# Performance work log

Hardware: AMD Instinct MI355X
Metric: run time of the kernel (lower is better)

## Reference

```python
import math
import jax, jax.numpy as jnp
import numpy as np

B, S, H, E, F = 4, 2048, 1024, 8, 2048
CAPACITY_FACTOR = 1.25


def setup_inputs() -> dict:
    key = jax.random.key(0)
    ks = jax.random.split(key, 5)
    x = jax.random.normal(ks[0], (B, S, H), dtype=jnp.float32)
    gate_w = jax.random.normal(ks[1], (H, E), dtype=jnp.float32) * 0.02
    w1 = jax.random.normal(ks[2], (E, H, F), dtype=jnp.float32) * 0.02
    w2 = jax.random.normal(ks[3], (E, F, H), dtype=jnp.float32) * 0.02
    w3 = jax.random.normal(ks[4], (E, H, F), dtype=jnp.float32) * 0.02
    return {"x": x, "gate_w": gate_w, "w1": w1, "w2": w2, "w3": w3}


def reference(x, gate_w, w1, w2, w3):
    b, s, h = x.shape
    T = b * s
    e = gate_w.shape[1]
    xf = x.reshape(T, h)                           # [T, H]
    logits = xf @ gate_w                           # [T, E]
    capacity = min(math.ceil(T / e * CAPACITY_FACTOR), T)
    # Expert-choice: each expert picks its top-`capacity` tokens.
    scores, idx = jax.lax.top_k(logits.T, capacity)  # both [E, C]
    # Per-expert softmax over the selected tokens (dim=0 of the column vector in torch == capacity axis here).
    weights = jax.nn.softmax(scores, axis=1)       # [E, C]
    gathered = xf[idx]                             # [E, C, H]
    # Grouped SwiGLU FFN
    a = jnp.einsum('ech,ehf->ecf', gathered, w1)
    g = jnp.einsum('ech,ehf->ecf', gathered, w3)
    hidden = jax.nn.silu(a) * g                    # [E, C, F]
    out_e = jnp.einsum('ecf,efh->ech', hidden, w2) # [E, C, H]
    out_e = out_e * weights[..., None]
    # Weighted scatter-add combine
    yf = jnp.zeros((T, h), dtype=x.dtype).at[idx.reshape(-1)].add(
        out_e.reshape(-1, h))
    return yf.reshape(b, s, h), jnp.float32(0.0)
```

## Files before the change

### kernel.cpp

```cpp
#include <hip/hip_runtime.h>
#include <stdint.h>

typedef unsigned short ushort_t;
typedef __bf16 bf16x8 __attribute__((ext_vector_type(8)));
typedef float f32x4 __attribute__((ext_vector_type(4)));

#define T_TOK 8192
#define HDIM  1024
#define EXP   8
#define FDIM  2048
#define CAP   1280

__device__ __forceinline__ unsigned short f2b(float f) {
  unsigned u = __float_as_uint(f);
  u = (u + 0x7fffu + ((u >> 16) & 1u)) >> 16;
  return (unsigned short)u;
}
__device__ __forceinline__ unsigned pk2(unsigned short lo, unsigned short hi) {
  return (unsigned)lo | ((unsigned)hi << 16);
}
__device__ __forceinline__ unsigned map_u(float f) {
  unsigned u = __float_as_uint(f);
  return (u & 0x80000000u) ? ~u : (u | 0x80000000u);
}
__device__ __forceinline__ float unmap_f(unsigned m) {
  unsigned u = (m & 0x80000000u) ? (m ^ 0x80000000u) : ~m;
  return __uint_as_float(u);
}
__device__ __forceinline__ void gl_lds16(const void* g, void* l) {
  __builtin_amdgcn_global_load_lds((__attribute__((address_space(1))) void*)g,
                                   (__attribute__((address_space(3))) void*)l,
                                   16, 0, 0);
}

__global__ void __launch_bounds__(256) gate_cast_k(
    const float* __restrict__ x, const float* __restrict__ gw,
    float* __restrict__ logitsT, ushort_t* __restrict__ xb)
{
  int wave = threadIdx.x >> 6, lane = threadIdx.x & 63;
  int t = blockIdx.x * 4 + wave;
  const float* xr = x + (size_t)t * HDIM;
  ushort_t* xbr = xb + (size_t)t * HDIM;
  float acc[8];
#pragma unroll
  for (int i = 0; i < 8; ++i) acc[i] = 0.f;
#pragma unroll
  for (int i = 0; i < 4; ++i) {
    int h0 = i * 256 + lane * 4;
    float4 xv = *(const float4*)(xr + h0);
    unsigned lo = pk2(f2b(xv.x), f2b(xv.y));
    unsigned hi = pk2(f2b(xv.z), f2b(xv.w));
    *(unsigned long long*)(xbr + h0) = (unsigned long long)lo | ((unsigned long long)hi << 32);
    float xs[4] = {xv.x, xv.y, xv.z, xv.w};
#pragma unroll
    for (int j = 0; j < 4; ++j) {
      const float4* g4 = (const float4*)(gw + (size_t)(h0 + j) * EXP);
      float4 glo = g4[0], ghi = g4[1];
      acc[0] += xs[j] * glo.x; acc[1] += xs[j] * glo.y;
      acc[2] += xs[j] * glo.z; acc[3] += xs[j] * glo.w;
      acc[4] += xs[j] * ghi.x; acc[5] += xs[j] * ghi.y;
      acc[6] += xs[j] * ghi.z; acc[7] += xs[j] * ghi.w;
    }
  }
#pragma unroll
  for (int off = 32; off > 0; off >>= 1) {
#pragma unroll
    for (int i = 0; i < 8; ++i) acc[i] += __shfl_xor(acc[i], off, 64);
  }
  if (lane == 0) {
#pragma unroll
    for (int i = 0; i < 8; ++i) logitsT[(size_t)i * T_TOK + t] = acc[i];
  }
}

__global__ void __launch_bounds__(256) select_k(
    const float* __restrict__ logitsT,
    unsigned* __restrict__ thr, int* __restrict__ needo, unsigned* __restrict__ umax)
{
  __shared__ int hist[4][256];
  __shared__ int ssum[256];
  __shared__ unsigned s_pref;
  __shared__ int s_rem;
  __shared__ unsigned smx[4];
  int e = blockIdx.x, tid = threadIdx.x;
  const float* base = logitsT + (size_t)e * T_TOK;

  unsigned m[32];
  unsigned mmax = 0;
#pragma unroll
  for (int i = 0; i < 32; ++i) {
    m[i] = map_u(base[tid + i * 256]);
    mmax = m[i] > mmax ? m[i] : mmax;
  }
#pragma unroll
  for (int off = 32; off > 0; off >>= 1) {
    unsigned o = __shfl_xor(mmax, off, 64);
    mmax = o > mmax ? o : mmax;
  }
  int lane = tid & 63, wv = tid >> 6;
  if (lane == 0) smx[wv] = mmax;
  if (tid == 0) { s_pref = 0; s_rem = CAP; }
  __syncthreads();
  if (tid == 0) {
    unsigned a = smx[0] > smx[1] ? smx[0] : smx[1];
    unsigned b = smx[2] > smx[3] ? smx[2] : smx[3];
    umax[e] = a > b ? a : b;
  }

  for (int r = 0; r < 4; ++r) {
#pragma unroll
    for (int w = 0; w < 4; ++w) hist[w][tid] = 0;
    __syncthreads();
    unsigned pref = s_pref;
    int rem = s_rem;
    int shift = 24 - 8 * r;
#pragma unroll
    for (int i = 0; i < 32; ++i) {
      unsigned u = m[i];
      bool ok = (r == 0) || ((u >> (shift + 8)) == (pref >> (shift + 8)));
      if (ok) atomicAdd(&hist[wv][(u >> shift) & 255], 1);
    }
    __syncthreads();
    ssum[tid] = hist[0][tid] + hist[1][tid] + hist[2][tid] + hist[3][tid];
    __syncthreads();
    for (int st = 1; st < 256; st <<= 1) {
      int add = (tid + st < 256) ? ssum[tid + st] : 0;
      __syncthreads();
      ssum[tid] += add;
      __syncthreads();
    }
    int above = (tid < 255) ? ssum[tid + 1] : 0;
    if (ssum[tid] >= rem && above < rem) {
      s_pref = pref | ((unsigned)tid << shift);
      s_rem = rem - above;
    }
    __syncthreads();
  }
  if (tid == 0) { thr[e] = s_pref; needo[e] = s_rem; }
}

__global__ void __launch_bounds__(256) emit_k(
    const float* __restrict__ logitsT,
    const unsigned* __restrict__ thr, const int* __restrict__ needv,
    const unsigned* __restrict__ umaxv,
    int* __restrict__ idxo, float* __restrict__ exo,
    int* __restrict__ cnt, int* __restrict__ tie, float* __restrict__ expsum,
    int* __restrict__ tok_cnt, int* __restrict__ tok_ent)
{
  int t = blockIdx.x * 256 + threadIdx.x;
  int lane = threadIdx.x & 63;
  int lc = 0;
  int ents[8];
#pragma unroll
  for (int e = 0; e < EXP; ++e) {
    float f = logitsT[(size_t)e * T_TOK + t];
    unsigned u = map_u(f);
    unsigned te = thr[e];
    float fm = unmap_f(umaxv[e]);
    float v = __expf(f - fm);
    bool sel = u > te;
    unsigned long long mask = __ballot(sel);
    int nsel = __popcll(mask);
    int base = 0;
    if (lane == 0 && nsel) base = atomicAdd(&cnt[e], nsel);
    base = __shfl(base, 0, 64);
    int slot = -1;
    if (sel) slot = base + __popcll(mask & ((1ull << lane) - 1ull));
    if (u == te) {
      int k = atomicAdd(&tie[e], 1);
      if (k < needv[e]) {
        slot = atomicAdd(&cnt[e], 1);
        atomicAdd(&expsum[e], v);
      }
    }
    if (slot >= 0) {
      idxo[e * CAP + slot] = t;
      exo[e * CAP + slot] = v;
      ents[lc++] = (e << 16) | slot;
    }
    float vs = sel ? v : 0.f;
#pragma unroll
    for (int off = 32; off > 0; off >>= 1) vs += __shfl_xor(vs, off, 64);
    if (lane == 0 && vs != 0.f) atomicAdd(&expsum[e], vs);
  }
  tok_cnt[t] = lc;
  for (int i = 0; i < lc; ++i) tok_ent[t * 8 + i] = ents[i];
}

__global__ void __launch_bounds__(256) transpose3_k(
    const float* __restrict__ w1, const float* __restrict__ w3, const float* __restrict__ w2,
    ushort_t* __restrict__ w1t, ushort_t* __restrict__ w3t, ushort_t* __restrict__ w2t)
{
  __shared__ float tile[64][65];
  int b = blockIdx.x;
  const float* in; ushort_t* out; int R, Cc;
  if (b < 4096)      { in = w1; out = w1t; R = HDIM; Cc = FDIM; }
  else if (b < 8192) { in = w3; out = w3t; R = HDIM; Cc = FDIM; b -= 4096; }
  else               { in = w2; out = w2t; R = FDIM; Cc = HDIM; b -= 8192; }
  int tilesC = Cc >> 6;
  int tilesPer = (R >> 6) * tilesC;
  int e = b / tilesPer;
  int tb = b - e * tilesPer;
  int rt = tb / tilesC, ct = tb - rt * tilesC;
  const float* src = in + (size_t)e * R * Cc;
  ushort_t* dst = out + (size_t)e * R * Cc;
  int tr = threadIdx.x >> 4, tc = threadIdx.x & 15;
#pragma unroll
  for (int it = 0; it < 4; ++it) {
    int r = (rt << 6) + (it << 4) + tr;
    int c = (ct << 6) + (tc << 2);
    float4 v = *(const float4*)(src + (size_t)r * Cc + c);
    tile[(it << 4) + tr][(tc << 2) + 0] = v.x;
    tile[(it << 4) + tr][(tc << 2) + 1] = v.y;
    tile[(it << 4) + tr][(tc << 2) + 2] = v.z;
    tile[(it << 4) + tr][(tc << 2) + 3] = v.w;
  }
  __syncthreads();
#pragma unroll
  for (int it = 0; it < 4; ++it) {
    int cl = (it << 4) + tr;
    int rl = tc << 2;
    unsigned lo = pk2(f2b(tile[rl + 0][cl]), f2b(tile[rl + 1][cl]));
    unsigned hi = pk2(f2b(tile[rl + 2][cl]), f2b(tile[rl + 3][cl]));
    unsigned long long v = (unsigned long long)lo | ((unsigned long long)hi << 32);
    *(unsigned long long*)(dst + (size_t)((ct << 6) + cl) * R + (rt << 6) + rl) = v;
  }
}

#define G1_STAGE(BB) \
  gl_lds16(pA0, lds + (BB)*12288 + (size_t)tid*8); \
  gl_lds16(pA1, lds + (BB)*12288 + 4096 + (size_t)tid*8); \
  gl_lds16(pB , lds + (BB)*12288 + 8192 + (size_t)tid*8);

#define G1_ITER(CB, PB, VM, PREF) { \
  asm volatile("s_waitcnt vmcnt(" VM ")" ::: "memory"); \
  __builtin_amdgcn_s_barrier(); \
  if (PREF) { G1_STAGE(PB); pA0 += 32; pA1 += 32; pB += 32; } \
  bf16x8 af[4], b1v[2], b3v[2]; \
  _Pragma("unroll") \
  for (int mi = 0; mi < 4; ++mi) af[mi] = *(const bf16x8*)(lds + (CB)*12288 + aoff[mi]); \
  _Pragma("unroll") \
  for (int nj = 0; nj < 2; ++nj) { \
    b1v[nj] = *(const bf16x8*)(lds + (CB)*12288 + b1off[nj]); \
    b3v[nj] = *(const bf16x8*)(lds + (CB)*12288 + b1off[nj] + 2048); } \
  __builtin_amdgcn_s_setprio(1); \
  _Pragma("unroll") \
  for (int mi = 0; mi < 4; ++mi) \
    _Pragma("unroll") \
    for (int nj = 0; nj < 2; ++nj) { \
      acc1[mi][nj] = __builtin_amdgcn_mfma_f32_16x16x32_bf16(af[mi], b1v[nj], acc1[mi][nj], 0, 0, 0); \
      acc3[mi][nj] = __builtin_amdgcn_mfma_f32_16x16x32_bf16(af[mi], b3v[nj], acc3[mi][nj], 0, 0, 0); } \
  __builtin_amdgcn_s_setprio(0); \
}

__global__ void __launch_bounds__(512) gemm1_swiglu_k(
    const ushort_t* __restrict__ xb,
    const ushort_t* __restrict__ w1t,
    const ushort_t* __restrict__ w3t,
    const int* __restrict__ idx,
    ushort_t* __restrict__ hidden)
{
  int bb = blockIdx.x;
  int b = (bb & 7) * 160 + (bb >> 3);
  int ft = b & 31; int t1 = b >> 5; int mt = t1 % 5; int e = t1 / 5;
  int f0 = ft * 64;

  __shared__ __bf16 lds[3 * 12288];

  int tid = threadIdx.x;
  int lane = tid & 63, wave = tid >> 6;
  int wm = wave >> 1;
  int wn = wave & 1;
  int l15 = lane & 15, quad = lane >> 4;

  int srow = tid >> 2;
  int chunk = tid & 3;
  int s_sw = (srow & 3) ^ ((srow >> 2) & 3);
  int g_chunk = ((chunk ^ s_sw) * 8);

  const int* idxe = idx + e * CAP + mt * 256;
  int tok0 = idxe[srow];
  int tok1 = idxe[srow + 128];
  const ushort_t* pA0 = xb + (size_t)tok0 * HDIM + g_chunk;
  const ushort_t* pA1 = xb + (size_t)tok1 * HDIM + g_chunk;
  const ushort_t* pB = (srow < 64)
      ? (w1t + ((size_t)e * FDIM + f0 + srow) * HDIM + g_chunk)
      : (w3t + ((size_t)e * FDIM + f0 + (srow - 64)) * HDIM + g_chunk);

  int aoff[4], b1off[2];
#pragma unroll
  for (int mi = 0; mi < 4; ++mi) {
    int R = wm * 64 + mi * 16 + l15;
    int sw = (R & 3) ^ ((R >> 2) & 3);
    aoff[mi] = R * 32 + ((quad ^ sw) * 8);
  }
#pragma unroll
  for (int nj = 0; nj < 2; ++nj) {
    int r1 = wn * 32 + nj * 16 + l15;
    int sw = (r1 & 3) ^ ((r1 >> 2) & 3);
    b1off[nj] = 8192 + r1 * 32 + ((quad ^ sw) * 8);
  }

  f32x4 acc1[4][2], acc3[4][2];
#pragma unroll
  for (int i = 0; i < 4; ++i)
#pragma unroll
    for (int j = 0; j < 2; ++j) {
      acc1[i][j] = (f32x4){0.f, 0.f, 0.f, 0.f};
      acc3[i][j] = (f32x4){0.f, 0.f, 0.f, 0.f};
    }

  G1_STAGE(0); pA0 += 32; pA1 += 32; pB += 32;
  G1_STAGE(1); pA0 += 32; pA1 += 32; pB += 32;

  for (int it = 0; it < 10; ++it) {
    G1_ITER(0, 2, "3", 1)
    G1_ITER(1, 0, "3", 1)
    G1_ITER(2, 1, "3", 1)
  }
  G1_ITER(0, 0, "3", 0)
  G1_ITER(1, 0, "0", 0)

  ushort_t* hb = hidden + ((size_t)e * CAP + mt * 256) * FDIM + f0;
#pragma unroll
  for (int mi = 0; mi < 4; ++mi)
#pragma unroll
    for (int nj = 0; nj < 2; ++nj)
#pragma unroll
      for (int r = 0; r < 4; ++r) {
        int row = wm * 64 + mi * 16 + quad * 4 + r;
        int col = wn * 32 + nj * 16 + l15;
        float v1 = acc1[mi][nj][r];
        float v3 = acc3[mi][nj][r];
        float s = (v1 / (1.f + __expf(-v1))) * v3;
        hb[(size_t)row * FDIM + col] = f2b(s);
      }
}

#define G2_STAGE(BB) \
  gl_lds16(pA, lds2 + (BB)*8192 + (size_t)tid*8); \
  gl_lds16(pB, lds2 + (BB)*8192 + 4096 + (size_t)tid*8);

#define G2_ITER(CB, PB, VM, PREF) { \
  asm volatile("s_waitcnt vmcnt(" VM ")" ::: "memory"); \
  __builtin_amdgcn_s_barrier(); \
  if (PREF) { G2_STAGE(PB); pA += 32; pB += 32; } \
  bf16x8 af[4], bf[2]; \
  _Pragma("unroll") \
  for (int mi = 0; mi < 4; ++mi) af[mi] = *(const bf16x8*)(lds2 + (CB)*8192 + aoff[mi]); \
  _Pragma("unroll") \
  for (int nj = 0; nj < 2; ++nj) bf[nj] = *(const bf16x8*)(lds2 + (CB)*8192 + boff[nj]); \
  __builtin_amdgcn_s_setprio(1); \
  _Pragma("unroll") \
  for (int mi = 0; mi < 4; ++mi) \
    _Pragma("unroll") \
    for (int nj = 0; nj < 2; ++nj) \
      acc[mi][nj] = __builtin_amdgcn_mfma_f32_16x16x32_bf16(af[mi], bf[nj], acc[mi][nj], 0, 0, 0); \
  __builtin_amdgcn_s_setprio(0); \
}

__global__ void __launch_bounds__(512) gemm2_k(
    const ushort_t* __restrict__ hidden,
    const ushort_t* __restrict__ w2t,
    const float* __restrict__ ex, const float* __restrict__ expsum,
    float* __restrict__ oute)
{
  int bb = blockIdx.x;
  int b = (bb & 7) * 80 + (bb >> 3);
  int nt = b & 7; int t1 = b >> 3; int mt = t1 % 10; int e = t1 / 10;

  __shared__ __bf16 lds2[3 * 8192];
  __shared__ float wgts[128];

  int tid = threadIdx.x;
  int lane = tid & 63, wave = tid >> 6;
  int wm = wave >> 2;
  int wn = wave & 3;
  int l15 = lane & 15, quad = lane >> 4;

  if (tid < 128) wgts[tid] = ex[e * CAP + mt * 128 + tid] / expsum[e];

  int srow = tid >> 2;
  int chunk = tid & 3;
  int s_sw = (srow & 3) ^ ((srow >> 2) & 3);
  int g_chunk = ((chunk ^ s_sw) * 8);

  const ushort_t* pA = hidden + ((size_t)e * CAP + mt * 128 + srow) * FDIM + g_chunk;
  const ushort_t* pB = w2t + ((size_t)e * HDIM + nt * 128 + srow) * FDIM + g_chunk;

  int aoff[4], boff[2];
#pragma unroll
  for (int mi = 0; mi < 4; ++mi) {
    int R = wm * 64 + mi * 16 + l15;
    int sw = (R & 3) ^ ((R >> 2) & 3);
    aoff[mi] = R * 32 + ((quad ^ sw) * 8);
  }
#pragma unroll
  for (int nj = 0; nj < 2; ++nj) {
    int r = wn * 32 + nj * 16 + l15;
    int sw = (r & 3) ^ ((r >> 2) & 3);
    boff[nj] = 4096 + r * 32 + ((quad ^ sw) * 8);
  }

  f32x4 acc[4][2];
#pragma unroll
  for (int i = 0; i < 4; ++i)
#pragma unroll
    for (int j = 0; j < 2; ++j) acc[i][j] = (f32x4){0.f, 0.f, 0.f, 0.f};

  G2_STAGE(0); pA += 32; pB += 32;
  G2_STAGE(1); pA += 32; pB += 32;

  for (int it = 0; it < 20; ++it) {
    G2_ITER(0, 2, "2", 1)
    G2_ITER(1, 0, "2", 1)
    G2_ITER(2, 1, "2", 1)
  }
  G2_ITER(0, 2, "2", 1)
  G2_ITER(1, 0, "2", 1)
  G2_ITER(2, 0, "2", 0)
  G2_ITER(0, 0, "0", 0)

  float* ob = oute + ((size_t)e * CAP + mt * 128) * HDIM + nt * 128;
#pragma unroll
  for (int mi = 0; mi < 4; ++mi)
#pragma unroll
    for (int nj = 0; nj < 2; ++nj)
#pragma unroll
      for (int r = 0; r < 4; ++r) {
        int row = wm * 64 + mi * 16 + quad * 4 + r;
        int col = wn * 32 + nj * 16 + l15;
        ob[(size_t)row * HDIM + col] = acc[mi][nj][r] * wgts[row];
      }
}

__global__ void __launch_bounds__(256) combine_k(
    const float* __restrict__ oute,
    const int* __restrict__ tok_cnt, const int* __restrict__ tok_ent,
    float* __restrict__ y)
{
  int t = blockIdx.x;
  int c = threadIdx.x * 4;
  int n = tok_cnt[t];
  float4 acc = {0.f, 0.f, 0.f, 0.f};
  for (int i = 0; i < n; ++i) {
    int ent = tok_ent[t * 8 + i];
    int e = ent >> 16, slot = ent & 0xffff;
    float4 v = *(const float4*)(oute + (((size_t)e * CAP + slot) << 10) + c);
    acc.x += v.x; acc.y += v.y; acc.z += v.z; acc.w += v.w;
  }
  *(float4*)(y + ((size_t)t << 10) + c) = acc;
}

extern "C" void kernel_launch(void* const* d_in, const int* in_sizes, int n_in,
                              void* d_out, int out_size, void* d_ws, size_t ws_size,
                              hipStream_t stream)
{
  const float* x  = (const float*)d_in[0];
  const float* gw = (const float*)d_in[1];
  const float* w1 = (const float*)d_in[2];
  const float* w2 = (const float*)d_in[3];
  const float* w3 = (const float*)d_in[4];
  float* y = (float*)d_out;

  char* ws = (char*)d_ws;
  float*    logitsT = (float*)(ws + 0x0);
  int*      idx     = (int*)(ws + 0x40000);
  float*    exo     = (float*)(ws + 0x4A000);
  unsigned* thr    = (unsigned*)(ws + 0x54000);
  int*      need   = (int*)(ws + 0x54020);
  unsigned* umax   = (unsigned*)(ws + 0x54040);
  int*      cnt    = (int*)(ws + 0x54060);
  int*      tie    = (int*)(ws + 0x54080);
  float*    expsum = (float*)(ws + 0x540A0);
  int*      tok_cnt = (int*)(ws + 0x55000);
  int*      tok_ent = (int*)(ws + 0x5D000);
  ushort_t* xb     = (ushort_t*)(ws + 0xA0000);
  ushort_t* w1t    = (ushort_t*)(ws + 0x10A0000);
  ushort_t* w3t    = (ushort_t*)(ws + 0x30A0000);
  ushort_t* w2t    = (ushort_t*)(ws + 0x50A0000);
  ushort_t* hid    = (ushort_t*)(ws + 0x70A0000);
  float*    oute   = (float*)(ws + 0x10A0000);

  size_t yelems = (size_t)T_TOK * HDIM;
  if ((size_t)out_size > yelems)
    hipMemsetAsync((char*)d_out + yelems * 4, 0, ((size_t)out_size - yelems) * 4, stream);
  hipMemsetAsync(ws + 0x54000, 0, 256, stream);

  transpose3_k<<<3 * 4096, 256, 0, stream>>>(w1, w3, w2, w1t, w3t, w2t);
  gate_cast_k<<<T_TOK / 4, 256, 0, stream>>>(x, gw, logitsT, xb);
  select_k<<<EXP, 256, 0, stream>>>(logitsT, thr, need, umax);
  emit_k<<<T_TOK / 256, 256, 0, stream>>>(logitsT, thr, need, umax, idx, exo, cnt, tie, expsum, tok_cnt, tok_ent);
  gemm1_swiglu_k<<<EXP * 5 * 32, 512, 0, stream>>>(xb, w1t, w3t, idx, hid);
  gemm2_k<<<EXP * 10 * 8, 512, 0, stream>>>(hid, w2t, exo, expsum, oute);
  combine_k<<<T_TOK, 256, 0, stream>>>(oute, tok_cnt, tok_ent, y);
}
```

Measured before the change: 468.9 us.

## Merge transpose and gate kernels; shrink gemm1 tiles to 128 rows

Folds the weight transpose/cast kernel and the gate/cast kernel into one launch, with block ranges selecting the role. This removes a launch and lets the two independent prep stages overlap. The SwiGLU gemm1 moves from 512-thread blocks on 256-token tiles to 256-thread blocks on 128-token tiles, with a smaller LDS footprint and twice the grid. The block-to-tile mapping is also changed to interleave experts. Smaller tiles mean more weight reloads per token but higher occupancy and more blocks to spread across CUs.

After: 475.5 us. Within noise of the previous version (+1.4%).

```diff
diff --git a/kernel.cpp b/kernel.cpp
--- a/kernel.cpp
+++ b/kernel.cpp
@@ -33,43 +33,83 @@
                                    16, 0, 0);
 }
 
-__global__ void __launch_bounds__(256) gate_cast_k(
+__global__ void __launch_bounds__(256) prep_k(
+    const float* __restrict__ w1, const float* __restrict__ w3, const float* __restrict__ w2,
+    ushort_t* __restrict__ w1t, ushort_t* __restrict__ w3t, ushort_t* __restrict__ w2t,
     const float* __restrict__ x, const float* __restrict__ gw,
     float* __restrict__ logitsT, ushort_t* __restrict__ xb)
 {
-  int wave = threadIdx.x >> 6, lane = threadIdx.x & 63;
-  int t = blockIdx.x * 4 + wave;
-  const float* xr = x + (size_t)t * HDIM;
-  ushort_t* xbr = xb + (size_t)t * HDIM;
-  float acc[8];
-#pragma unroll
-  for (int i = 0; i < 8; ++i) acc[i] = 0.f;
-#pragma unroll
-  for (int i = 0; i < 4; ++i) {
-    int h0 = i * 256 + lane * 4;
-    float4 xv = *(const float4*)(xr + h0);
-    unsigned lo = pk2(f2b(xv.x), f2b(xv.y));
-    unsigned hi = pk2(f2b(xv.z), f2b(xv.w));
-    *(unsigned long long*)(xbr + h0) = (unsigned long long)lo | ((unsigned long long)hi << 32);
-    float xs[4] = {xv.x, xv.y, xv.z, xv.w};
-#pragma unroll
-    for (int j = 0; j < 4; ++j) {
-      const float4* g4 = (const float4*)(gw + (size_t)(h0 + j) * EXP);
-      float4 glo = g4[0], ghi = g4[1];
-      acc[0] += xs[j] * glo.x; acc[1] += xs[j] * glo.y;
-      acc[2] += xs[j] * glo.z; acc[3] += xs[j] * glo.w;
-      acc[4] += xs[j] * ghi.x; acc[5] += xs[j] * ghi.y;
-      acc[6] += xs[j] * ghi.z; acc[7] += xs[j] * ghi.w;
-    }
-  }
-#pragma unroll
-  for (int off = 32; off > 0; off >>= 1) {
-#pragma unroll
-    for (int i = 0; i < 8; ++i) acc[i] += __shfl_xor(acc[i], off, 64);
-  }
-  if (lane == 0) {
-#pragma unroll
-    for (int i = 0; i < 8; ++i) logitsT[(size_t)i * T_TOK + t] = acc[i];
+  __shared__ float tile[64][65];
+  int bb = blockIdx.x;
+  if (bb >= 12288) {
+    int wave = threadIdx.x >> 6, lane = threadIdx.x & 63;
+    int t = (bb - 12288) * 4 + wave;
+    const float* xr = x + (size_t)t * HDIM;
+    ushort_t* xbr = xb + (size_t)t * HDIM;
+    float acc[8];
+#pragma unroll
+    for (int i = 0; i < 8; ++i) acc[i] = 0.f;
+#pragma unroll
+    for (int i = 0; i < 4; ++i) {
+      int h0 = i * 256 + lane * 4;
+      float4 xv = *(const float4*)(xr + h0);
+      unsigned lo = pk2(f2b(xv.x), f2b(xv.y));
+      unsigned hi = pk2(f2b(xv.z), f2b(xv.w));
+      *(unsigned long long*)(xbr + h0) = (unsigned long long)lo | ((unsigned long long)hi << 32);
+      float xs[4] = {xv.x, xv.y, xv.z, xv.w};
+#pragma unroll
+      for (int j = 0; j < 4; ++j) {
+        const float4* g4 = (const float4*)(gw + (size_t)(h0 + j) * EXP);
+        float4 glo = g4[0], ghi = g4[1];
+        acc[0] += xs[j] * glo.x; acc[1] += xs[j] * glo.y;
+        acc[2] += xs[j] * glo.z; acc[3] += xs[j] * glo.w;
+        acc[4] += xs[j] * ghi.x; acc[5] += xs[j] * ghi.y;
+        acc[6] += xs[j] * ghi.z; acc[7] += xs[j] * ghi.w;
+      }
+    }
+#pragma unroll
+    for (int off = 32; off > 0; off >>= 1) {
+#pragma unroll
+      for (int i = 0; i < 8; ++i) acc[i] += __shfl_xor(acc[i], off, 64);
+    }
+    if (lane == 0) {
+#pragma unroll
+      for (int i = 0; i < 8; ++i) logitsT[(size_t)i * T_TOK + t] = acc[i];
+    }
+    return;
+  }
+  int b = bb;
+  const float* in; ushort_t* out; int R, Cc;
+  if (b < 4096)      { in = w1; out = w1t; R = HDIM; Cc = FDIM; }
+  else if (b < 8192) { in = w3; out = w3t; R = HDIM; Cc = FDIM; b -= 4096; }
+  else               { in = w2; out = w2t; R = FDIM; Cc = HDIM; b -= 8192; }
+  int tilesC = Cc >> 6;
+  int tilesPer = (R >> 6) * tilesC;
+  int e = b / tilesPer;
+  int tb = b - e * tilesPer;
+  int rt = tb / tilesC, ct = tb - rt * tilesC;
+  const float* src = in + (size_t)e * R * Cc;
+  ushort_t* dst = out + (size_t)e * R * Cc;
+  int tr = threadIdx.x >> 4, tc = threadIdx.x & 15;
+#pragma unroll
+  for (int it = 0; it < 4; ++it) {
+    int r = (rt << 6) + (it << 4) + tr;
+    int c = (ct << 6) + (tc << 2);
+    float4 v = *(const float4*)(src + (size_t)r * Cc + c);
+    tile[(it << 4) + tr][(tc << 2) + 0] = v.x;
+    tile[(it << 4) + tr][(tc << 2) + 1] = v.y;
+    tile[(it << 4) + tr][(tc << 2) + 2] = v.z;
+    tile[(it << 4) + tr][(tc << 2) + 3] = v.w;
+  }
+  __syncthreads();
+#pragma unroll
+  for (int it = 0; it < 4; ++it) {
+    int cl = (it << 4) + tr;
+    int rl = tc << 2;
+    unsigned lo = pk2(f2b(tile[rl + 0][cl]), f2b(tile[rl + 1][cl]));
+    unsigned hi = pk2(f2b(tile[rl + 2][cl]), f2b(tile[rl + 3][cl]));
+    unsigned long long v = (unsigned long long)lo | ((unsigned long long)hi << 32);
+    *(unsigned long long*)(dst + (size_t)((ct << 6) + cl) * R + (rt << 6) + rl) = v;
   }
 }
 
@@ -187,62 +227,25 @@
   for (int i = 0; i < lc; ++i) tok_ent[t * 8 + i] = ents[i];
 }
 
-__global__ void __launch_bounds__(256) transpose3_k(
-    const float* __restrict__ w1, const float* __restrict__ w3, const float* __restrict__ w2,
-    ushort_t* __restrict__ w1t, ushort_t* __restrict__ w3t, ushort_t* __restrict__ w2t)
-{
-  __shared__ float tile[64][65];
-  int b = blockIdx.x;
-  const float* in; ushort_t* out; int R, Cc;
-  if (b < 4096)      { in = w1; out = w1t; R = HDIM; Cc = FDIM; }
-  else if (b < 8192) { in = w3; out = w3t; R = HDIM; Cc = FDIM; b -= 4096; }
-  else               { in = w2; out = w2t; R = FDIM; Cc = HDIM; b -= 8192; }
-  int tilesC = Cc >> 6;
-  int tilesPer = (R >> 6) * tilesC;
-  int e = b / tilesPer;
-  int tb = b - e * tilesPer;
-  int rt = tb / tilesC, ct = tb - rt * tilesC;
-  const float* src = in + (size_t)e * R * Cc;
-  ushort_t* dst = out + (size_t)e * R * Cc;
-  int tr = threadIdx.x >> 4, tc = threadIdx.x & 15;
-#pragma unroll
-  for (int it = 0; it < 4; ++it) {
-    int r = (rt << 6) + (it << 4) + tr;
-    int c = (ct << 6) + (tc << 2);
-    float4 v = *(const float4*)(src + (size_t)r * Cc + c);
-    tile[(it << 4) + tr][(tc << 2) + 0] = v.x;
-    tile[(it << 4) + tr][(tc << 2) + 1] = v.y;
-    tile[(it << 4) + tr][(tc << 2) + 2] = v.z;
-    tile[(it << 4) + tr][(tc << 2) + 3] = v.w;
-  }
-  __syncthreads();
-#pragma unroll
-  for (int it = 0; it < 4; ++it) {
-    int cl = (it << 4) + tr;
-    int rl = tc << 2;
-    unsigned lo = pk2(f2b(tile[rl + 0][cl]), f2b(tile[rl + 1][cl]));
-    unsigned hi = pk2(f2b(tile[rl + 2][cl]), f2b(tile[rl + 3][cl]));
-    unsigned long long v = (unsigned long long)lo | ((unsigned long long)hi << 32);
-    *(unsigned long long*)(dst + (size_t)((ct << 6) + cl) * R + (rt << 6) + rl) = v;
-  }
-}
-
 #define G1_STAGE(BB) \
-  gl_lds16(pA0, lds + (BB)*12288 + (size_t)tid*8); \
-  gl_lds16(pA1, lds + (BB)*12288 + 4096 + (size_t)tid*8); \
-  gl_lds16(pB , lds + (BB)*12288 + 8192 + (size_t)tid*8);
-
-#define G1_ITER(CB, PB, VM, PREF) { \
+  gl_lds16(pA0, lds + (BB)*8192 + (size_t)tid*8); \
+  gl_lds16(pA1, lds + (BB)*8192 + 2048 + (size_t)tid*8); \
+  gl_lds16(pB0, lds + (BB)*8192 + 4096 + (size_t)tid*8); \
+  gl_lds16(pB1, lds + (BB)*8192 + 6144 + (size_t)tid*8);
+
+#define G1_ADV { pA0 += 32; pA1 += 32; pB0 += 32; pB1 += 32; }
+
+#define G1_ITER(CB, VM, PREF) { \
   asm volatile("s_waitcnt vmcnt(" VM ")" ::: "memory"); \
   __builtin_amdgcn_s_barrier(); \
-  if (PREF) { G1_STAGE(PB); pA0 += 32; pA1 += 32; pB += 32; } \
+  if (PREF) { G1_STAGE(((CB) + 2) % 3); G1_ADV; } \
   bf16x8 af[4], b1v[2], b3v[2]; \
   _Pragma("unroll") \
-  for (int mi = 0; mi < 4; ++mi) af[mi] = *(const bf16x8*)(lds + (CB)*12288 + aoff[mi]); \
+  for (int mi = 0; mi < 4; ++mi) af[mi] = *(const bf16x8*)(lds + (CB)*8192 + aoff[mi]); \
   _Pragma("unroll") \
   for (int nj = 0; nj < 2; ++nj) { \
-    b1v[nj] = *(const bf16x8*)(lds + (CB)*12288 + b1off[nj]); \
-    b3v[nj] = *(const bf16x8*)(lds + (CB)*12288 + b1off[nj] + 2048); } \
+    b1v[nj] = *(const bf16x8*)(lds + (CB)*8192 + b1off[nj]); \
+    b3v[nj] = *(const bf16x8*)(lds + (CB)*8192 + b1off[nj] + 2048); } \
   __builtin_amdgcn_s_setprio(1); \
   _Pragma("unroll") \
   for (int mi = 0; mi < 4; ++mi) \
@@ -253,7 +256,7 @@
   __builtin_amdgcn_s_setprio(0); \
 }
 
-__global__ void __launch_bounds__(512) gemm1_swiglu_k(
+__global__ void __launch_bounds__(256) gemm1_swiglu_k(
     const ushort_t* __restrict__ xb,
     const ushort_t* __restrict__ w1t,
     const ushort_t* __restrict__ w3t,
@@ -261,11 +264,13 @@
     ushort_t* __restrict__ hidden)
 {
   int bb = blockIdx.x;
-  int b = (bb & 7) * 160 + (bb >> 3);
-  int ft = b & 31; int t1 = b >> 5; int mt = t1 % 5; int e = t1 / 5;
+  int e = bb & 7;
+  int k = bb >> 3;
+  int mt = k % 10;
+  int ft = k / 10;
   int f0 = ft * 64;
 
-  __shared__ __bf16 lds[3 * 12288];
+  __shared__ __bf16 lds[3 * 8192];
 
   int tid = threadIdx.x;
   int lane = tid & 63, wave = tid >> 6;
@@ -273,19 +278,18 @@
   int wn = wave & 1;
   int l15 = lane & 15, quad = lane >> 4;
 
-  int srow = tid >> 2;
-  int chunk = tid & 3;
-  int s_sw = (srow & 3) ^ ((srow >> 2) & 3);
-  int g_chunk = ((chunk ^ s_sw) * 8);
-
-  const int* idxe = idx + e * CAP + mt * 256;
-  int tok0 = idxe[srow];
-  int tok1 = idxe[srow + 128];
+  int r = tid >> 2;
+  int c = tid & 3;
+  int s_sw = (r & 3) ^ ((r >> 2) & 3);
+  int g_chunk = ((c ^ s_sw) * 8);
+
+  const int* idxe = idx + e * CAP + mt * 128;
+  int tok0 = idxe[r];
+  int tok1 = idxe[r + 64];
   const ushort_t* pA0 = xb + (size_t)tok0 * HDIM + g_chunk;
   const ushort_t* pA1 = xb + (size_t)tok1 * HDIM + g_chunk;
-  const ushort_t* pB = (srow < 64)
-      ? (w1t + ((size_t)e * FDIM + f0 + srow) * HDIM + g_chunk)
-      : (w3t + ((size_t)e * FDIM + f0 + (srow - 64)) * HDIM + g_chunk);
+  const ushort_t* pB0 = w1t + ((size_t)e * FDIM + f0 + r) * HDIM + g_chunk;
+  const ushort_t* pB1 = w3t + ((size_t)e * FDIM + f0 + r) * HDIM + g_chunk;
 
   int aoff[4], b1off[2];
 #pragma unroll
@@ -298,7 +302,7 @@
   for (int nj = 0; nj < 2; ++nj) {
     int r1 = wn * 32 + nj * 16 + l15;
     int sw = (r1 & 3) ^ ((r1 >> 2) & 3);
-    b1off[nj] = 8192 + r1 * 32 + ((quad ^ sw) * 8);
+    b1off[nj] = 4096 + r1 * 32 + ((quad ^ sw) * 8);
   }
 
   f32x4 acc1[4][2], acc3[4][2];
@@ -310,28 +314,28 @@
       acc3[i][j] = (f32x4){0.f, 0.f, 0.f, 0.f};
     }
 
-  G1_STAGE(0); pA0 += 32; pA1 += 32; pB += 32;
-  G1_STAGE(1); pA0 += 32; pA1 += 32; pB += 32;
+  G1_STAGE(0); G1_ADV;
+  G1_STAGE(1); G1_ADV;
 
   for (int it = 0; it < 10; ++it) {
-    G1_ITER(0, 2, "3", 1)
-    G1_ITER(1, 0, "3", 1)
-    G1_ITER(2, 1, "3", 1)
-  }
-  G1_ITER(0, 0, "3", 0)
-  G1_ITER(1, 0, "0", 0)
-
-  ushort_t* hb = hidden + ((size_t)e * CAP + mt * 256) * FDIM + f0;
+    G1_ITER(0, "4", 1)
+    G1_ITER(1, "4", 1)
+    G1_ITER(2, "4", 1)
+  }
+  G1_ITER(0, "4", 0)
+  G1_ITER(1, "0", 0)
+
+  ushort_t* hb = hidden + ((size_t)e * CAP + mt * 128) * FDIM + f0;
 #pragma unroll
   for (int mi = 0; mi < 4; ++mi)
 #pragma unroll
     for (int nj = 0; nj < 2; ++nj)
 #pragma unroll
-      for (int r = 0; r < 4; ++r) {
-        int row = wm * 64 + mi * 16 + quad * 4 + r;
+      for (int rr = 0; rr < 4; ++rr) {
+        int row = wm * 64 + mi * 16 + quad * 4 + rr;
         int col = wn * 32 + nj * 16 + l15;
-        float v1 = acc1[mi][nj][r];
-        float v3 = acc3[mi][nj][r];
+        float v1 = acc1[mi][nj][rr];
+        float v3 = acc3[mi][nj][rr];
         float s = (v1 / (1.f + __expf(-v1))) * v3;
         hb[(size_t)row * FDIM + col] = f2b(s);
       }
@@ -397,9 +401,9 @@
   }
 #pragma unroll
   for (int nj = 0; nj < 2; ++nj) {
-    int r = wn * 32 + nj * 16 + l15;
-    int sw = (r & 3) ^ ((r >> 2) & 3);
-    boff[nj] = 4096 + r * 32 + ((quad ^ sw) * 8);
+    int r2 = wn * 32 + nj * 16 + l15;
+    int sw = (r2 & 3) ^ ((r2 >> 2) & 3);
+    boff[nj] = 4096 + r2 * 32 + ((quad ^ sw) * 8);
   }
 
   f32x4 acc[4][2];
@@ -427,10 +431,10 @@
 #pragma unroll
     for (int nj = 0; nj < 2; ++nj)
 #pragma unroll
-      for (int r = 0; r < 4; ++r) {
-        int row = wm * 64 + mi * 16 + quad * 4 + r;
+      for (int rr = 0; rr < 4; ++rr) {
+        int row = wm * 64 + mi * 16 + quad * 4 + rr;
         int col = wn * 32 + nj * 16 + l15;
-        ob[(size_t)row * HDIM + col] = acc[mi][nj][r] * wgts[row];
+        ob[(size_t)row * HDIM + col] = acc[mi][nj][rr] * wgts[row];
       }
 }
 
@@ -487,11 +491,10 @@
     hipMemsetAsync((char*)d_out + yelems * 4, 0, ((size_t)out_size - yelems) * 4, stream);
   hipMemsetAsync(ws + 0x54000, 0, 256, stream);
 
-  transpose3_k<<<3 * 4096, 256, 0, stream>>>(w1, w3, w2, w1t, w3t, w2t);
-  gate_cast_k<<<T_TOK / 4, 256, 0, stream>>>(x, gw, logitsT, xb);
+  prep_k<<<12288 + 2048, 256, 0, stream>>>(w1, w3, w2, w1t, w3t, w2t, x, gw, logitsT, xb);
   select_k<<<EXP, 256, 0, stream>>>(logitsT, thr, need, umax);
   emit_k<<<T_TOK / 256, 256, 0, stream>>>(logitsT, thr, need, umax, idx, exo, cnt, tie, expsum, tok_cnt, tok_ent);
-  gemm1_swiglu_k<<<EXP * 5 * 32, 512, 0, stream>>>(xb, w1t, w3t, idx, hid);
+  gemm1_swiglu_k<<<EXP * 10 * 32, 256, 0, stream>>>(xb, w1t, w3t, idx, hid);
   gemm2_k<<<EXP * 10 * 8, 512, 0, stream>>>(hid, w2t, exo, expsum, oute);
   combine_k<<<T_TOK, 256, 0, stream>>>(oute, tok_cnt, tok_ent, y);
 }
```

## Merge weight transpose and gate/cast kernels; transpose four tiles per block

Applied to the files above, without the earlier changes.

Combines the weight transpose-to-bf16 kernel and the gate-logit/x-cast kernel into one launch, with block ranges dispatched to each role. Each transpose block now handles four 64x64 tiles, issuing all global loads before the LDS transposes so more memory requests are in flight. The goal is to cut one launch plus its tail and raise memory-level parallelism. In exchange each transpose block holds more registers and has fewer blocks to spread the work. Some loop variables in gemm2 are also renamed with no effect.

Result: no change. 465.9 us (-0.6%).

```diff
diff --git a/kernel.cpp b/kernel.cpp
--- a/kernel.cpp
+++ b/kernel.cpp
@@ -33,44 +33,102 @@
                                    16, 0, 0);
 }
 
-__global__ void __launch_bounds__(256) gate_cast_k(
+#define PREP_LOAD(VV, G) { \
+  _Pragma("unroll") \
+  for (int it = 0; it < 4; ++it) { \
+    int r = (rt << 6) + (it << 4) + tr; \
+    int c = ((ct0 + (G)) << 6) + (tc << 2); \
+    VV[it] = *(const float4*)(src + (size_t)r * Cc + c); \
+  } }
+
+#define PREP_DO(VV, G) { \
+  __syncthreads(); \
+  _Pragma("unroll") \
+  for (int it = 0; it < 4; ++it) { \
+    tile[(it << 4) + tr][(tc << 2) + 0] = VV[it].x; \
+    tile[(it << 4) + tr][(tc << 2) + 1] = VV[it].y; \
+    tile[(it << 4) + tr][(tc << 2) + 2] = VV[it].z; \
+    tile[(it << 4) + tr][(tc << 2) + 3] = VV[it].w; \
+  } \
+  __syncthreads(); \
+  _Pragma("unroll") \
+  for (int it = 0; it < 4; ++it) { \
+    int cl = (it << 4) + tr; \
+    int rl = tc << 2; \
+    unsigned lo = pk2(f2b(tile[rl + 0][cl]), f2b(tile[rl + 1][cl])); \
+    unsigned hi = pk2(f2b(tile[rl + 2][cl]), f2b(tile[rl + 3][cl])); \
+    unsigned long long v = (unsigned long long)lo | ((unsigned long long)hi << 32); \
+    *(unsigned long long*)(dst + (size_t)(((ct0 + (G)) << 6) + cl) * R + (rt << 6) + rl) = v; \
+  } }
+
+__global__ void __launch_bounds__(256) prep_k(
+    const float* __restrict__ w1, const float* __restrict__ w3, const float* __restrict__ w2,
+    ushort_t* __restrict__ w1t, ushort_t* __restrict__ w3t, ushort_t* __restrict__ w2t,
     const float* __restrict__ x, const float* __restrict__ gw,
     float* __restrict__ logitsT, ushort_t* __restrict__ xb)
 {
-  int wave = threadIdx.x >> 6, lane = threadIdx.x & 63;
-  int t = blockIdx.x * 4 + wave;
-  const float* xr = x + (size_t)t * HDIM;
-  ushort_t* xbr = xb + (size_t)t * HDIM;
-  float acc[8];
-#pragma unroll
-  for (int i = 0; i < 8; ++i) acc[i] = 0.f;
-#pragma unroll
-  for (int i = 0; i < 4; ++i) {
-    int h0 = i * 256 + lane * 4;
-    float4 xv = *(const float4*)(xr + h0);
-    unsigned lo = pk2(f2b(xv.x), f2b(xv.y));
-    unsigned hi = pk2(f2b(xv.z), f2b(xv.w));
-    *(unsigned long long*)(xbr + h0) = (unsigned long long)lo | ((unsigned long long)hi << 32);
-    float xs[4] = {xv.x, xv.y, xv.z, xv.w};
-#pragma unroll
-    for (int j = 0; j < 4; ++j) {
-      const float4* g4 = (const float4*)(gw + (size_t)(h0 + j) * EXP);
-      float4 glo = g4[0], ghi = g4[1];
-      acc[0] += xs[j] * glo.x; acc[1] += xs[j] * glo.y;
-      acc[2] += xs[j] * glo.z; acc[3] += xs[j] * glo.w;
-      acc[4] += xs[j] * ghi.x; acc[5] += xs[j] * ghi.y;
-      acc[6] += xs[j] * ghi.z; acc[7] += xs[j] * ghi.w;
-    }
-  }
-#pragma unroll
-  for (int off = 32; off > 0; off >>= 1) {
-#pragma unroll
-    for (int i = 0; i < 8; ++i) acc[i] += __shfl_xor(acc[i], off, 64);
-  }
-  if (lane == 0) {
-#pragma unroll
-    for (int i = 0; i < 8; ++i) logitsT[(size_t)i * T_TOK + t] = acc[i];
-  }
+  __shared__ float tile[64][65];
+  int bb = blockIdx.x;
+  if (bb >= 3072) {
+    int wave = threadIdx.x >> 6, lane = threadIdx.x & 63;
+    int t = (bb - 3072) * 4 + wave;
+    const float* xr = x + (size_t)t * HDIM;
+    ushort_t* xbr = xb + (size_t)t * HDIM;
+    float acc[8];
+#pragma unroll
+    for (int i = 0; i < 8; ++i) acc[i] = 0.f;
+#pragma unroll
+    for (int i = 0; i < 4; ++i) {
+      int h0 = i * 256 + lane * 4;
+      float4 xv = *(const float4*)(xr + h0);
+      unsigned lo = pk2(f2b(xv.x), f2b(xv.y));
+      unsigned hi = pk2(f2b(xv.z), f2b(xv.w));
+      *(unsigned long long*)(xbr + h0) = (unsigned long long)lo | ((unsigned long long)hi << 32);
+      float xs[4] = {xv.x, xv.y, xv.z, xv.w};
+#pragma unroll
+      for (int j = 0; j < 4; ++j) {
+        const float4* g4 = (const float4*)(gw + (size_t)(h0 + j) * EXP);
+        float4 glo = g4[0], ghi = g4[1];
+        acc[0] += xs[j] * glo.x; acc[1] += xs[j] * glo.y;
+        acc[2] += xs[j] * glo.z; acc[3] += xs[j] * glo.w;
+        acc[4] += xs[j] * ghi.x; acc[5] += xs[j] * ghi.y;
+        acc[6] += xs[j] * ghi.z; acc[7] += xs[j] * ghi.w;
+      }
+    }
+#pragma unroll
+    for (int off = 32; off > 0; off >>= 1) {
+#pragma unroll
+      for (int i = 0; i < 8; ++i) acc[i] += __shfl_xor(acc[i], off, 64);
+    }
+    if (lane == 0) {
+#pragma unroll
+      for (int i = 0; i < 8; ++i) logitsT[(size_t)i * T_TOK + t] = acc[i];
+    }
+    return;
+  }
+  int b = bb;
+  const float* in; ushort_t* out; int R, Cc;
+  if (b < 1024)      { in = w1; out = w1t; R = HDIM; Cc = FDIM; }
+  else if (b < 2048) { in = w3; out = w3t; R = HDIM; Cc = FDIM; b -= 1024; }
+  else               { in = w2; out = w2t; R = FDIM; Cc = HDIM; b -= 2048; }
+  int colgroups = Cc >> 8;
+  int e = b >> 7;
+  int tb = b & 127;
+  int rt = tb / colgroups;
+  int ct0 = (tb % colgroups) * 4;
+  const float* src = in + (size_t)e * R * Cc;
+  ushort_t* dst = out + (size_t)e * R * Cc;
+  int tr = threadIdx.x >> 4, tc = threadIdx.x & 15;
+
+  float4 v0[4], v1[4], v2[4], v3[4];
+  PREP_LOAD(v0, 0)
+  PREP_LOAD(v1, 1)
+  PREP_LOAD(v2, 2)
+  PREP_LOAD(v3, 3)
+  PREP_DO(v0, 0)
+  PREP_DO(v1, 1)
+  PREP_DO(v2, 2)
+  PREP_DO(v3, 3)
 }
 
 __global__ void __launch_bounds__(256) select_k(
@@ -187,46 +245,6 @@
   for (int i = 0; i < lc; ++i) tok_ent[t * 8 + i] = ents[i];
 }
 
-__global__ void __launch_bounds__(256) transpose3_k(
-    const float* __restrict__ w1, const float* __restrict__ w3, const float* __restrict__ w2,
-    ushort_t* __restrict__ w1t, ushort_t* __restrict__ w3t, ushort_t* __restrict__ w2t)
-{
-  __shared__ float tile[64][65];
-  int b = blockIdx.x;
-  const float* in; ushort_t* out; int R, Cc;
-  if (b < 4096)      { in = w1; out = w1t; R = HDIM; Cc = FDIM; }
-  else if (b < 8192) { in = w3; out = w3t; R = HDIM; Cc = FDIM; b -= 4096; }
-  else               { in = w2; out = w2t; R = FDIM; Cc = HDIM; b -= 8192; }
-  int tilesC = Cc >> 6;
-  int tilesPer = (R >> 6) * tilesC;
-  int e = b / tilesPer;
-  int tb = b - e * tilesPer;
-  int rt = tb / tilesC, ct = tb - rt * tilesC;
-  const float* src = in + (size_t)e * R * Cc;
-  ushort_t* dst = out + (size_t)e * R * Cc;
-  int tr = threadIdx.x >> 4, tc = threadIdx.x & 15;
-#pragma unroll
-  for (int it = 0; it < 4; ++it) {
-    int r = (rt << 6) + (it << 4) + tr;
-    int c = (ct << 6) + (tc << 2);
-    float4 v = *(const float4*)(src + (size_t)r * Cc + c);
-    tile[(it << 4) + tr][(tc << 2) + 0] = v.x;
-    tile[(it << 4) + tr][(tc << 2) + 1] = v.y;
-    tile[(it << 4) + tr][(tc << 2) + 2] = v.z;
-    tile[(it << 4) + tr][(tc << 2) + 3] = v.w;
-  }
-  __syncthreads();
-#pragma unroll
-  for (int it = 0; it < 4; ++it) {
-    int cl = (it << 4) + tr;
-    int rl = tc << 2;
-    unsigned lo = pk2(f2b(tile[rl + 0][cl]), f2b(tile[rl + 1][cl]));
-    unsigned hi = pk2(f2b(tile[rl + 2][cl]), f2b(tile[rl + 3][cl]));
-    unsigned long long v = (unsigned long long)lo | ((unsigned long long)hi << 32);
-    *(unsigned long long*)(dst + (size_t)((ct << 6) + cl) * R + (rt << 6) + rl) = v;
-  }
-}
-
 #define G1_STAGE(BB) \
   gl_lds16(pA0, lds + (BB)*12288 + (size_t)tid*8); \
   gl_lds16(pA1, lds + (BB)*12288 + 4096 + (size_t)tid*8); \
@@ -397,9 +415,9 @@
   }
 #pragma unroll
   for (int nj = 0; nj < 2; ++nj) {
-    int r = wn * 32 + nj * 16 + l15;
-    int sw = (r & 3) ^ ((r >> 2) & 3);
-    boff[nj] = 4096 + r * 32 + ((quad ^ sw) * 8);
+    int r2 = wn * 32 + nj * 16 + l15;
+    int sw = (r2 & 3) ^ ((r2 >> 2) & 3);
+    boff[nj] = 4096 + r2 * 32 + ((quad ^ sw) * 8);
   }
 
   f32x4 acc[4][2];
@@ -427,10 +445,10 @@
 #pragma unroll
     for (int nj = 0; nj < 2; ++nj)
 #pragma unroll
-      for (int r = 0; r < 4; ++r) {
-        int row = wm * 64 + mi * 16 + quad * 4 + r;
+      for (int rr = 0; rr < 4; ++rr) {
+        int row = wm * 64 + mi * 16 + quad * 4 + rr;
         int col = wn * 32 + nj * 16 + l15;
-        ob[(size_t)row * HDIM + col] = acc[mi][nj][r] * wgts[row];
+        ob[(size_t)row * HDIM + col] = acc[mi][nj][rr] * wgts[row];
       }
 }
 
@@ -487,8 +505,7 @@
     hipMemsetAsync((char*)d_out + yelems * 4, 0, ((size_t)out_size - yelems) * 4, stream);
   hipMemsetAsync(ws + 0x54000, 0, 256, stream);
 
-  transpose3_k<<<3 * 4096, 256, 0, stream>>>(w1, w3, w2, w1t, w3t, w2t);
-  gate_cast_k<<<T_TOK / 4, 256, 0, stream>>>(x, gw, logitsT, xb);
+  prep_k<<<3072 + 2048, 256, 0, stream>>>(w1, w3, w2, w1t, w3t, w2t, x, gw, logitsT, xb);
   select_k<<<EXP, 256, 0, stream>>>(logitsT, thr, need, umax);
   emit_k<<<T_TOK / 256, 256, 0, stream>>>(logitsT, thr, need, umax, idx, exo, cnt, tie, expsum, tok_cnt, tok_ent);
   gemm1_swiglu_k<<<EXP * 5 * 32, 512, 0, stream>>>(xb, w1t, w3t, idx, hid);
```
